# Performance work log

Hardware: AMD Instinct MI355X
Metric: run time of the kernel (lower is better)

Reference implementation:

```python
import jax, jax.numpy as jnp
import numpy as np

B, S, C, H, L = 256, 8, 8, 501, 56


def _lin_init(k, out_dim, in_dim):
    k1, k2 = jax.random.split(k)
    s = 1.0 / np.sqrt(in_dim)
    w = jax.random.uniform(k1, (out_dim, in_dim), jnp.float32, -s, s)
    b = jax.random.uniform(k2, (out_dim,), jnp.float32, -s, s)
    return w, b


def setup_inputs() -> dict:
    key = jax.random.key(0)
    ks = jax.random.split(key, 12)
    lin1_w, lin1_b = _lin_init(ks[0], H, L)
    av_w1, av_b1 = _lin_init(ks[1], 2 * H, H)
    av_w2, av_b2 = _lin_init(ks[2], C, 2 * H)
    ae_w1, ae_b1 = _lin_init(ks[3], 4 * H, 2 * H)
    ae_w2, ae_b2 = _lin_init(ks[4], 1, 4 * H)
    gate_w, gate_b = _lin_init(ks[5], H, H)
    map_w, map_b = _lin_init(ks[6], H, H)
    gru_w_ih, gru_b_ih = _lin_init(ks[7], 3 * H, C)
    gru_w_hh, gru_b_hh = _lin_init(ks[8], 3 * H, H)
    z = jax.random.normal(ks[9], (B, L), jnp.float32)
    dep_graph = jax.random.uniform(ks[10], (B, S, S), jnp.float32)
    node_encoding = jax.random.uniform(ks[11], (B, S, C), jnp.float32)
    return dict(z=z, dep_graph=dep_graph, node_encoding=node_encoding,
                lin1_w=lin1_w, lin1_b=lin1_b,
                av_w1=av_w1, av_b1=av_b1, av_w2=av_w2, av_b2=av_b2,
                ae_w1=ae_w1, ae_b1=ae_b1, ae_w2=ae_w2, ae_b2=ae_b2,
                gate_w=gate_w, gate_b=gate_b, map_w=map_w, map_b=map_b,
                gru_w_ih=gru_w_ih, gru_w_hh=gru_w_hh,
                gru_b_ih=gru_b_ih, gru_b_hh=gru_b_hh)


def _forward(z, dep_graph, node_encoding,
             lin1_w, lin1_b, av_w1, av_b1, av_w2, av_b2,
             ae_w1, ae_b1, ae_w2, ae_b2, gate_w, gate_b, map_w, map_b,
             gru_w_ih, gru_w_hh, gru_b_ih, gru_b_hh):
    b, s, _ = dep_graph.shape
    h = lin1_w.shape[0]

    def gru(x, hid):  # torch GRUCell math
        gi = x @ gru_w_ih.T + gru_b_ih
        gh = hid @ gru_w_hh.T + gru_b_hh
        i_r, i_z, i_n = jnp.split(gi, 3, axis=-1)
        h_r, h_z, h_n = jnp.split(gh, 3, axis=-1)
        r = jax.nn.sigmoid(i_r + h_r)
        zz = jax.nn.sigmoid(i_z + h_z)
        n = jnp.tanh(i_n + r * h_n)
        return (1.0 - zz) * n + zz * hid

    pos = jnp.arange(s)

    def outer_step(carry, xs):
        graph_state, nhs = carry  # (B,H), (B,S,H)
        index, x, dep_row = xs    # scalar, (B,C), (B,S)
        logits = jax.nn.softmax(
            jax.nn.relu(graph_state @ av_w1.T + av_b1) @ av_w2.T + av_b2, axis=-1)
        # index==0: gru seeded with graph_state; otherwise zero hidden
        h0 = jnp.where(index == 0, graph_state, jnp.zeros_like(graph_state))
        hv0 = gru(x, h0)

        def inner_step(c, j):
            hv, nhs_c, edge_row = c
            active = j < index  # replicate range(index-1, -1, -1)
            hidden_j = nhs_c[:, j]
            e = jnp.concatenate([hv, hidden_j], axis=1)
            edge = (jax.nn.relu(e @ ae_w1.T + ae_b1) @ ae_w2.T + ae_b2)[:, 0]
            edge_row = edge_row.at[:, j].set(jnp.where(active, edge, 0.0))
            # ancestors: dep_graph[:, index] with positions < j zeroed
            anc = dep_row * (pos >= j).astype(dep_row.dtype)
            a = (nhs_c * anc[:, :, None]).reshape(b * s, h)
            h_in = (jax.nn.sigmoid(a @ gate_w.T + gate_b) *
                    (a @ map_w.T + map_b)).reshape(b, s, h).sum(axis=1)
            hv_new = gru(x, h_in)
            hv = jnp.where(active, hv_new, hv)
            nhs_c = nhs_c.at[:, index].set(jnp.where(active, hv_new, nhs_c[:, index]))
            return (hv, nhs_c, edge_row), None

        (hv, nhs, edge_row), _ = jax.lax.scan(
            inner_step, (hv0, nhs, jnp.zeros((b, s), dep_graph.dtype)),
            jnp.arange(s - 1, -1, -1))
        nhs = nhs.at[:, index].set(hv)
        return (hv, nhs), (logits, edge_row)

    graph_state0 = z @ lin1_w.T + lin1_b
    nhs0 = jnp.zeros((b, s, h), z.dtype)
    (_, _), (gen_enc, gen_dep) = jax.lax.scan(
        outer_step, (graph_state0, nhs0),
        (jnp.arange(s), node_encoding.transpose(1, 0, 2), dep_graph.transpose(1, 0, 2)))
    return gen_dep.transpose(1, 0, 2), gen_enc.transpose(1, 0, 2)


def reference(z, dep_graph, node_encoding,
              lin1_w, lin1_b, av_w1, av_b1, av_w2, av_b2,
              ae_w1, ae_b1, ae_w2, ae_b2, gate_w, gate_b, map_w, map_b,
              gru_w_ih, gru_w_hh, gru_b_ih, gru_b_hh):
    return _forward(z, dep_graph, node_encoding,
                    lin1_w, lin1_b, av_w1, av_b1, av_w2, av_b2,
                    ae_w1, ae_b1, ae_w2, ae_b2, gate_w, gate_b, map_w, map_b,
                    gru_w_ih, gru_w_hh, gru_b_ih, gru_b_hh)
```

## Files before the change

kernel.cpp:

```cpp
#include <hip/hip_runtime.h>
#include <math.h>

constexpr int NB  = 256;
constexpr int NS  = 8;
constexpr int NC  = 8;
constexpr int NH  = 501;
constexpr int NL  = 56;
constexpr int NH2 = 1002;
constexpr int NH3 = 1503;
constexpr int NH4 = 2004;
constexpr int KT  = 1536;
constexpr int KE  = 512;
constexpr int HV  = 512 * 256;

typedef unsigned short u16;
typedef short bf16x8v __attribute__((ext_vector_type(8)));
typedef _Float16 f16x8v __attribute__((ext_vector_type(8)));
typedef _Float16 f16x4v __attribute__((ext_vector_type(4)));
typedef float f32x4 __attribute__((ext_vector_type(4)));

__device__ __forceinline__ float sigf(float x) { return 1.0f / (1.0f + __expf(-x)); }
__device__ __forceinline__ float tanh2(float x) { return 2.0f * sigf(2.0f * x) - 1.0f; }

__device__ __forceinline__ u16 f2bf(float x) {
  union { float f; unsigned u; } c; c.f = x;
  unsigned r = (c.u + 0x7fffu + ((c.u >> 16) & 1u)) >> 16;
  return (u16)r;
}
__device__ __forceinline__ float bf2f(u16 h) {
  union { float f; unsigned u; } c; c.u = ((unsigned)h) << 16; return c.f;
}

__device__ __forceinline__ void async_copy16(const void* g, void* l) {
  __builtin_amdgcn_global_load_lds(
      (const __attribute__((address_space(1))) unsigned int*)g,
      (__attribute__((address_space(3))) unsigned int*)l, 16, 0, 0);
}

__device__ __forceinline__ f32x4 mfma_bf(bf16x8v a, bf16x8v b, f32x4 c) {
  return __builtin_amdgcn_mfma_f32_16x16x32_bf16(a, b, c, 0, 0, 0);
}
__device__ __forceinline__ f32x4 mfma_h(f16x8v a, f16x8v b, f32x4 c) {
  return __builtin_amdgcn_mfma_f32_16x16x32_f16(a, b, c, 0, 0, 0);
}

__device__ __forceinline__ void storeTrio(u16* __restrict__ T, int b, int h0, const float v[4]) {
  size_t base = (size_t)b * KT;
  if (h0 + 3 < NH) {
    ushort4 hi4, lo4;
    u16 hi, lo;
    hi = f2bf(v[0]); lo = f2bf(v[0] - bf2f(hi)); hi4.x = hi; lo4.x = lo;
    hi = f2bf(v[1]); lo = f2bf(v[1] - bf2f(hi)); hi4.y = hi; lo4.y = lo;
    hi = f2bf(v[2]); lo = f2bf(v[2] - bf2f(hi)); hi4.z = hi; lo4.z = lo;
    hi = f2bf(v[3]); lo = f2bf(v[3] - bf2f(hi)); hi4.w = hi; lo4.w = lo;
    *(ushort4*)&T[base + h0]        = hi4;
    *(ushort4*)&T[base + 512 + h0]  = lo4;
    *(ushort4*)&T[base + 1024 + h0] = hi4;
  } else {
    for (int r = 0; r < 4; ++r) {
      int h = h0 + r;
      if (h < NH) {
        u16 hi = f2bf(v[r]); u16 lo = f2bf(v[r] - bf2f(hi));
        T[base + h] = hi; T[base + 512 + h] = lo; T[base + 1024 + h] = hi;
      }
    }
  }
}


__global__ __launch_bounds__(256) void kZero4(float4* __restrict__ p, int n4) {
  int i = blockIdx.x * 256 + threadIdx.x;
  if (i < n4) p[i] = make_float4(0.f, 0.f, 0.f, 0.f);
}

__global__ __launch_bounds__(256) void kInit0(float* __restrict__ out0,
                                              const float* __restrict__ ae_b2) {
  int e = blockIdx.x * 256 + threadIdx.x;
  int b = e >> 6, r = e & 63;
  int i = r >> 3, jj = r & 7;
  out0[b * 64 + i * 8 + jj] = (jj < i) ? ae_b2[0] : 0.f;
}

__global__ __launch_bounds__(256) void kPack(
    const float* __restrict__ gate_w, const float* __restrict__ map_w,
    const float* __restrict__ w_hh, const float* __restrict__ av_w1,
    const float* __restrict__ ae_w1,
    u16* __restrict__ Wgm, u16* __restrict__ Whh, u16* __restrict__ Wav1,
    u16* __restrict__ Wr3, _Float16* __restrict__ Wl) {
  int r = blockIdx.x;
  for (int k = threadIdx.x; k < 512; k += 256) {
    if (r < 5632) {
      float v = 0.f; u16* dst; int rr;
      if (r < 1024) {
        int h = (r < 512) ? r : r - 512;
        if (h < NH && k < NH) v = (r < 512) ? gate_w[h * NH + k] : map_w[h * NH + k];
        dst = Wgm; rr = r;
      } else if (r < 2560) {
        rr = r - 1024; int g = rr >> 9, h = rr & 511;
        if (h < NH && k < NH) v = w_hh[((size_t)g * NH + h) * NH + k];
        dst = Whh;
      } else if (r < 3584) {
        rr = r - 2560;
        if (rr < NH2 && k < NH) v = av_w1[(size_t)rr * NH + k];
        dst = Wav1;
      } else {
        rr = r - 3584;
        if (rr < NH4 && k < NH) v = ae_w1[(size_t)rr * NH2 + NH + k];
        dst = Wr3;
      }
      u16 hi = f2bf(v); u16 lo = f2bf(v - bf2f(hi));
      dst[(size_t)rr * KT + k] = hi;
      dst[(size_t)rr * KT + 512 + k] = hi;
      dst[(size_t)rr * KT + 1024 + k] = lo;
    } else {
      int m = r - 5632; float v = 0.f;
      if (m < NH4 && k < NH) v = ae_w1[(size_t)m * NH2 + k];
      Wl[(size_t)m * KE + k] = (_Float16)v;
    }
  }
}

__global__ __launch_bounds__(256) void kLin1(const float* __restrict__ z,
                                             const float* __restrict__ w,
                                             const float* __restrict__ bias,
                                             float* __restrict__ g0, u16* __restrict__ GS0) {
  int b = blockIdx.x;
  const float* zr = z + (size_t)b * NL;
  for (int h = threadIdx.x; h < NH; h += 256) {
    const float* wr = w + (size_t)h * NL;
    float acc = bias[h];
#pragma unroll
    for (int l = 0; l < NL; ++l) acc += zr[l] * wr[l];
    g0[h * NB + b] = acc;
    u16 hi = f2bf(acc), lo = f2bf(acc - bf2f(hi));
    GS0[(size_t)b * KT + h] = hi;
    GS0[(size_t)b * KT + 512 + h] = lo;
    GS0[(size_t)b * KT + 1024 + h] = hi;
  }
}

__global__ __launch_bounds__(256) void kGiAll(const float* __restrict__ ne,
                                              const float* __restrict__ w_ih,
                                              const float* __restrict__ b_ih,
                                              float* __restrict__ gi,
                                              float* __restrict__ giT) {
  int r = blockIdx.x, b = threadIdx.x;
  int g = (r >= NH2) ? 2 : ((r >= NH) ? 1 : 0);
  int h = r - g * NH;
  float wv[8];
#pragma unroll
  for (int c = 0; c < 8; ++c) wv[c] = w_ih[r * NC + c];
  float bb = b_ih[r];
  for (int idx = 0; idx < 8; ++idx) {
    float acc = bb;
#pragma unroll
    for (int c = 0; c < 8; ++c) acc += ne[b * 64 + idx * 8 + c] * wv[c];
    gi[((size_t)idx * NH3 + r) * NB + b] = acc;
    giT[((size_t)idx * NB + b) * KT + g * 512 + h] = acc;
  }
}


__global__ __launch_bounds__(256) void kGMw(
    const u16* __restrict__ Wgm, const u16* __restrict__ Bsrc, int mode,
    int index, int j, const float* __restrict__ dep,
    const float* __restrict__ gate_b, const float* __restrict__ map_b,
    const float* __restrict__ Pcj, const float* __restrict__ Qcj,
    float* __restrict__ RS, float* __restrict__ hinF, u16* __restrict__ hinT,
    float* __restrict__ PcO, float* __restrict__ QcO) {
  __shared__ f32x4 red[4 * 4 * 64];
  const int b = blockIdx.x, t = threadIdx.x, w = t >> 6, l = t & 63;
  const int quad = l >> 4, lan = l & 15;
  const int ht = b & 31, ct = b >> 5;
  const u16* Ag = Wgm + (size_t)(ht * 16 + lan) * KT;
  const u16* Am = Wgm + (size_t)(512 + ht * 16 + lan) * KT;
  const u16* B0 = Bsrc + (size_t)(ct * 32 + lan) * KT;
  const u16* B1 = Bsrc + (size_t)(ct * 32 + 16 + lan) * KT;
  const int kb = w * 384 + quad * 8;
  f32x4 a0 = {0.f,0.f,0.f,0.f}, a1 = a0, a2 = a0, a3 = a0;
#pragma unroll 4
  for (int ks = 0; ks < 12; ++ks) {
    int k = kb + ks * 32;
    bf16x8v bg = *(const bf16x8v*)&B0[k];
    bf16x8v bh = *(const bf16x8v*)&B1[k];
    bf16x8v ag = *(const bf16x8v*)&Ag[k];
    bf16x8v am = *(const bf16x8v*)&Am[k];
    a0 = mfma_bf(ag, bg, a0); a1 = mfma_bf(ag, bh, a1);
    a2 = mfma_bf(am, bg, a2); a3 = mfma_bf(am, bh, a3);
  }
  red[(w * 4 + 0) * 64 + l] = a0;
  red[(w * 4 + 1) * 64 + l] = a1;
  red[(w * 4 + 2) * 64 + l] = a2;
  red[(w * 4 + 3) * 64 + l] = a3;
  __syncthreads();
  if (w < 2) {
    int ns = w;
    f32x4 G = red[(0 * 4 + ns) * 64 + l] + red[(1 * 4 + ns) * 64 + l] +
              red[(2 * 4 + ns) * 64 + l] + red[(3 * 4 + ns) * 64 + l];
    f32x4 M = red[(0 * 4 + 2 + ns) * 64 + l] + red[(1 * 4 + 2 + ns) * 64 + l] +
              red[(2 * 4 + 2 + ns) * 64 + l] + red[(3 * 4 + 2 + ns) * 64 + l];
    int c = ct * 32 + ns * 16 + lan;
    int h0 = ht * 16 + quad * 4;
    if (mode == 1) {
#pragma unroll
      for (int reg = 0; reg < 4; ++reg) {
        int h = h0 + reg;
        if (h < NH) { PcO[h * NB + c] = G[reg]; QcO[h * NB + c] = M[reg]; }
      }
    } else {
      float dj = dep[c * 64 + index * 8 + j];
      float di = dep[c * 64 + index * 8 + index];
      float cnt = (float)(7 - (index - j));
      float vout[4];
#pragma unroll
      for (int reg = 0; reg < 4; ++reg) {
        int h = h0 + reg; float v = 0.f;
        if (h < NH) {
          float gb = gate_b[h], mb = map_b[h];
          float kbv = sigf(gb) * mb;
          float fj = sigf(dj * Pcj[h * NB + c] + gb) * (dj * Qcj[h * NB + c] + mb);
          float rs = RS[h * NB + c] + fj;
          RS[h * NB + c] = rs;
          float fi = sigf(di * G[reg] + gb) * (di * M[reg] + mb);
          v = rs + fi + cnt * kbv;
          hinF[h * NB + c] = v;
        }
        vout[reg] = v;
      }
      storeTrio(hinT, c, h0, vout);
    }
  }
}

__global__ __launch_bounds__(256) void kHHw(
    const u16* __restrict__ Whh, const u16* __restrict__ Bsrc,
    const float* __restrict__ hidF, const float* __restrict__ gi,
    const float* __restrict__ b_hh,
    u16* __restrict__ dstT, _Float16* __restrict__ XeSlot) {
  __shared__ f32x4 red[4 * 6 * 64];
  const int b = blockIdx.x, t = threadIdx.x, w = t >> 6, l = t & 63;
  const int quad = l >> 4, lan = l & 15;
  const int ht = b & 31, ct = b >> 5;
  const u16* Ar = Whh + (size_t)(ht * 16 + lan) * KT;
  const u16* Az = Whh + (size_t)(512 + ht * 16 + lan) * KT;
  const u16* An = Whh + (size_t)(1024 + ht * 16 + lan) * KT;
  const u16* B0 = Bsrc + (size_t)(ct * 32 + lan) * KT;
  const u16* B1 = Bsrc + (size_t)(ct * 32 + 16 + lan) * KT;
  const int kb = w * 384 + quad * 8;
  f32x4 r0 = {0.f,0.f,0.f,0.f}, r1 = r0, z0 = r0, z1 = r0, n0 = r0, n1 = r0;
#pragma unroll 4
  for (int ks = 0; ks < 12; ++ks) {
    int k = kb + ks * 32;
    bf16x8v bg = *(const bf16x8v*)&B0[k];
    bf16x8v bh = *(const bf16x8v*)&B1[k];
    bf16x8v ar = *(const bf16x8v*)&Ar[k];
    bf16x8v az = *(const bf16x8v*)&Az[k];
    bf16x8v an = *(const bf16x8v*)&An[k];
    r0 = mfma_bf(ar, bg, r0); r1 = mfma_bf(ar, bh, r1);
    z0 = mfma_bf(az, bg, z0); z1 = mfma_bf(az, bh, z1);
    n0 = mfma_bf(an, bg, n0); n1 = mfma_bf(an, bh, n1);
  }
  red[(w * 6 + 0) * 64 + l] = r0;
  red[(w * 6 + 1) * 64 + l] = r1;
  red[(w * 6 + 2) * 64 + l] = z0;
  red[(w * 6 + 3) * 64 + l] = z1;
  red[(w * 6 + 4) * 64 + l] = n0;
  red[(w * 6 + 5) * 64 + l] = n1;
  __syncthreads();
  if (w < 2) {
    int ns = w;
    f32x4 Rr = red[(0 * 6 + 0 + ns) * 64 + l] + red[(1 * 6 + 0 + ns) * 64 + l] +
               red[(2 * 6 + 0 + ns) * 64 + l] + red[(3 * 6 + 0 + ns) * 64 + l];
    f32x4 Rz = red[(0 * 6 + 2 + ns) * 64 + l] + red[(1 * 6 + 2 + ns) * 64 + l] +
               red[(2 * 6 + 2 + ns) * 64 + l] + red[(3 * 6 + 2 + ns) * 64 + l];
    f32x4 Rn = red[(0 * 6 + 4 + ns) * 64 + l] + red[(1 * 6 + 4 + ns) * 64 + l] +
               red[(2 * 6 + 4 + ns) * 64 + l] + red[(3 * 6 + 4 + ns) * 64 + l];
    int c = ct * 32 + ns * 16 + lan;
    int h0 = ht * 16 + quad * 4;
    float vout[4];
#pragma unroll
    for (int reg = 0; reg < 4; ++reg) {
      int h = h0 + reg; float v = 0.f;
      if (h < NH) {
        float ir = gi[h * NB + c];
        float iz = gi[(NH + h) * NB + c];
        float inn = gi[(2 * NH + h) * NB + c];
        float rr = sigf(ir + Rr[reg] + b_hh[h]);
        float zz = sigf(iz + Rz[reg] + b_hh[NH + h]);
        float nn = tanh2(inn + rr * (Rn[reg] + b_hh[2 * NH + h]));
        float hd = hidF[h * NB + c];
        v = (1.f - zz) * nn + zz * hd;
      }
      vout[reg] = v;
    }
    storeTrio(dstT, c, h0, vout);
    if (XeSlot) {
      if (h0 + 3 < NH) {
        f16x4v xv; xv[0] = (_Float16)vout[0]; xv[1] = (_Float16)vout[1];
        xv[2] = (_Float16)vout[2]; xv[3] = (_Float16)vout[3];
        *(f16x4v*)&XeSlot[(size_t)c * KE + h0] = xv;
      } else {
        for (int reg = 0; reg < 4; ++reg)
          if (h0 + reg < NH) XeSlot[(size_t)c * KE + h0 + reg] = (_Float16)vout[reg];
      }
    }
  }
}

__global__ __launch_bounds__(256) void kPRO(
    int index, const float* __restrict__ dep,
    const float* __restrict__ gate_b, const float* __restrict__ map_b,
    const float* __restrict__ Pcj, const float* __restrict__ Qcj,
    float* __restrict__ RS, float* __restrict__ hinF, u16* __restrict__ hinT,
    const float* __restrict__ giT, const float* __restrict__ b_hh,
    _Float16* __restrict__ Xe0) {
  const int b = blockIdx.x, t = threadIdx.x;
  const int j = index - 1;
  const float cnt = (float)(7 - (index - j));
  if (b < 251) {
#pragma unroll
    for (int hh = 0; hh < 2; ++hh) {
      int h = 2 * b + hh;
      if (h < NH) {
        int c = t;
        float gb = gate_b[h], mb = map_b[h];
        float kbv = sigf(gb) * mb;
        float dj = dep[c * 64 + index * 8 + j];
        float fj = sigf(dj * Pcj[h * NB + c] + gb) * (dj * Qcj[h * NB + c] + mb);
        RS[h * NB + c] = fj;
        float v = fj + kbv + cnt * kbv;
        hinF[h * NB + c] = v;
        u16 hi = f2bf(v), lo = f2bf(v - bf2f(hi));
        hinT[(size_t)c * KT + h] = hi;
        hinT[(size_t)c * KT + 512 + h] = lo;
        hinT[(size_t)c * KT + 1024 + h] = hi;
      }
    }
  }
  {
    int c = b;
    const float* g = giT + ((size_t)index * NB + c) * KT;
    for (int h = t; h < NH; h += 256) {
      float rr = sigf(g[h] + b_hh[h]);
      float zz = sigf(g[512 + h] + b_hh[NH + h]);
      float nn = tanh2(g[1024 + h] + rr * b_hh[2 * NH + h]);
      Xe0[(size_t)c * KE + h] = (_Float16)((1.f - zz) * nn);
    }
  }
}


__global__ __launch_bounds__(256) void kR(const u16* __restrict__ Wr3,
                                          const u16* __restrict__ Bsrc,
                                          _Float16* __restrict__ R) {
  __shared__ u16 sA[2][128 * 32];
  __shared__ u16 sB[2][128 * 32];
  const int t = threadIdx.x, w = t >> 6, l = t & 63, quad = l >> 4, lan = l & 15;
  const int mB = blockIdx.x * 128, nB0 = blockIdx.y * 128;
  const int qs = quad ^ ((lan >> 1) & 3);
  const int sseg = (l & 3) ^ ((l >> 3) & 3);
  const u16 *gA0, *gA1, *gB0, *gB1;
  {
    int r0 = (w * 2 + 0) * 16 + (l >> 2), r1 = (w * 2 + 1) * 16 + (l >> 2);
    gA0 = Wr3 + (size_t)(mB + r0) * KT + sseg * 8;
    gA1 = Wr3 + (size_t)(mB + r1) * KT + sseg * 8;
    gB0 = Bsrc + (size_t)(nB0 + r0) * KT + sseg * 8;
    gB1 = Bsrc + (size_t)(nB0 + r1) * KT + sseg * 8;
  }
  f32x4 acc[2][8];
#pragma unroll
  for (int mt = 0; mt < 2; ++mt)
#pragma unroll
    for (int ns = 0; ns < 8; ++ns) acc[mt][ns] = (f32x4){0.f,0.f,0.f,0.f};
  async_copy16(gA0, &sA[0][(w * 2 + 0) * 512]);
  async_copy16(gA1, &sA[0][(w * 2 + 1) * 512]);
  async_copy16(gB0, &sB[0][(w * 2 + 0) * 512]);
  async_copy16(gB1, &sB[0][(w * 2 + 1) * 512]);
  for (int c = 0; c < 48; ++c) {
    __syncthreads();
    if (c + 1 < 48) {
      int nb = (c + 1) & 1, off = (c + 1) * 32;
      async_copy16(gA0 + off, &sA[nb][(w * 2 + 0) * 512]);
      async_copy16(gA1 + off, &sA[nb][(w * 2 + 1) * 512]);
      async_copy16(gB0 + off, &sB[nb][(w * 2 + 0) * 512]);
      async_copy16(gB1 + off, &sB[nb][(w * 2 + 1) * 512]);
    }
    const u16* bufA = sA[c & 1];
    const u16* bufB = sB[c & 1];
    bf16x8v av[2];
#pragma unroll
    for (int mt = 0; mt < 2; ++mt)
      av[mt] = *(const bf16x8v*)&bufA[(w * 32 + mt * 16 + lan) * 32 + qs * 8];
#pragma unroll
    for (int ns = 0; ns < 8; ++ns) {
      bf16x8v bv = *(const bf16x8v*)&bufB[(ns * 16 + lan) * 32 + qs * 8];
#pragma unroll
      for (int mt = 0; mt < 2; ++mt) acc[mt][ns] = mfma_bf(av[mt], bv, acc[mt][ns]);
    }
  }
#pragma unroll
  for (int ns = 0; ns < 8; ++ns) {
    int col = nB0 + ns * 16 + lan;
#pragma unroll
    for (int mt = 0; mt < 2; ++mt) {
      int m0 = mB + w * 32 + mt * 16 + quad * 4;
      f16x4v rv;
#pragma unroll
      for (int reg = 0; reg < 4; ++reg) rv[reg] = (_Float16)acc[mt][ns][reg];
      *(f16x4v*)&R[(size_t)col * 2048 + m0] = rv;
    }
  }
}

__global__ __launch_bounds__(256) void kEdge(const _Float16* __restrict__ Wl,
                                             const _Float16* __restrict__ Xe,
                                             const _Float16* __restrict__ R,
                                             const float* __restrict__ ae_b1,
                                             const float* __restrict__ ae_w2,
                                             float* __restrict__ out0) {
  __shared__ u16 sA[2][128 * 32];
  __shared__ u16 sB[2][128 * 32];
  __shared__ float shW[4][8][16];
  const int t = threadIdx.x, w = t >> 6, l = t & 63, quad = l >> 4, lan = l & 15;
  const int mB = blockIdx.x * 128, nB0 = blockIdx.y * 128;
  const int qs = quad ^ ((lan >> 1) & 3);
  const int sseg = (l & 3) ^ ((l >> 3) & 3);
  int sid = blockIdx.y >> 1;
  int idec = 1, bse = 0;
  while (sid >= bse + idec) { bse += idec; idec++; }
  int jdec = idec - 1 - (sid - bse);
  const _Float16 *gA0, *gA1, *gB0, *gB1;
  {
    int r0 = (w * 2 + 0) * 16 + (l >> 2), r1 = (w * 2 + 1) * 16 + (l >> 2);
    gA0 = Wl + (size_t)(mB + r0) * KE + sseg * 8;
    gA1 = Wl + (size_t)(mB + r1) * KE + sseg * 8;
    gB0 = Xe + (size_t)(nB0 + r0) * KE + sseg * 8;
    gB1 = Xe + (size_t)(nB0 + r1) * KE + sseg * 8;
  }
  f32x4 acc[2][8];
#pragma unroll
  for (int mt = 0; mt < 2; ++mt)
#pragma unroll
    for (int ns = 0; ns < 8; ++ns) acc[mt][ns] = (f32x4){0.f,0.f,0.f,0.f};
  async_copy16(gA0, &sA[0][(w * 2 + 0) * 512]);
  async_copy16(gA1, &sA[0][(w * 2 + 1) * 512]);
  async_copy16(gB0, &sB[0][(w * 2 + 0) * 512]);
  async_copy16(gB1, &sB[0][(w * 2 + 1) * 512]);
  for (int c = 0; c < 16; ++c) {
    __syncthreads();
    if (c + 1 < 16) {
      int nb = (c + 1) & 1, off = (c + 1) * 32;
      async_copy16(gA0 + off, &sA[nb][(w * 2 + 0) * 512]);
      async_copy16(gA1 + off, &sA[nb][(w * 2 + 1) * 512]);
      async_copy16(gB0 + off, &sB[nb][(w * 2 + 0) * 512]);
      async_copy16(gB1 + off, &sB[nb][(w * 2 + 1) * 512]);
    }
    const u16* bufA = sA[c & 1];
    const u16* bufB = sB[c & 1];
    f16x8v av[2];
#pragma unroll
    for (int mt = 0; mt < 2; ++mt)
      av[mt] = *(const f16x8v*)&bufA[(w * 32 + mt * 16 + lan) * 32 + qs * 8];
#pragma unroll
    for (int ns = 0; ns < 8; ++ns) {
      f16x8v bv = *(const f16x8v*)&bufB[(ns * 16 + lan) * 32 + qs * 8];
#pragma unroll
      for (int mt = 0; mt < 2; ++mt) acc[mt][ns] = mfma_h(av[mt], bv, acc[mt][ns]);
    }
  }
  float b1v[2][4], w2v[2][4];
#pragma unroll
  for (int mt = 0; mt < 2; ++mt) {
    int m0 = mB + w * 32 + mt * 16 + quad * 4;
#pragma unroll
    for (int reg = 0; reg < 4; ++reg) {
      int m = m0 + reg;
      b1v[mt][reg] = (m < NH4) ? ae_b1[m] : 0.f;
      w2v[mt][reg] = (m < NH4) ? ae_w2[m] : 0.f;
    }
  }
#pragma unroll
  for (int ns = 0; ns < 8; ++ns) {
    int bcol = (nB0 + ns * 16 + lan) & 255;
    const _Float16* Rp = R + (size_t)(jdec * 256 + bcol) * 2048 + mB + w * 32;
    float s = 0.f;
#pragma unroll
    for (int mt = 0; mt < 2; ++mt) {
      f16x4v rv = *(const f16x4v*)&Rp[mt * 16 + quad * 4];
#pragma unroll
      for (int reg = 0; reg < 4; ++reg) {
        float v = acc[mt][ns][reg] + (float)rv[reg] + b1v[mt][reg];
        if (v > 0.f) s += v * w2v[mt][reg];
      }
    }
    s += __shfl_xor(s, 16);
    s += __shfl_xor(s, 32);
    if (quad == 0) shW[w][ns][lan] = s;
  }
  __syncthreads();
  if (t < 128) {
    int ns = t >> 4, ln = t & 15;
    float tot = shW[0][ns][ln] + shW[1][ns][ln] + shW[2][ns][ln] + shW[3][ns][ln];
    int b = (nB0 + ln + ns * 16) & 255;
    atomicAdd(&out0[b * 64 + idec * 8 + jdec], tot);
  }
}

__global__ __launch_bounds__(256) void kLogA(const u16* __restrict__ Wav1,
                                             const u16* __restrict__ Bsrc,
                                             const float* __restrict__ av_b1,
                                             _Float16* __restrict__ t1) {
  __shared__ u16 sA[2][128 * 32];
  __shared__ u16 sB[2][128 * 32];
  const int t = threadIdx.x, w = t >> 6, l = t & 63, quad = l >> 4, lan = l & 15;
  const int mB = blockIdx.x * 128, nB0 = blockIdx.y * 128;
  const int qs = quad ^ ((lan >> 1) & 3);
  const int sseg = (l & 3) ^ ((l >> 3) & 3);
  const u16 *gA0, *gA1, *gB0, *gB1;
  {
    int r0 = (w * 2 + 0) * 16 + (l >> 2), r1 = (w * 2 + 1) * 16 + (l >> 2);
    gA0 = Wav1 + (size_t)(mB + r0) * KT + sseg * 8;
    gA1 = Wav1 + (size_t)(mB + r1) * KT + sseg * 8;
    gB0 = Bsrc + (size_t)(nB0 + r0) * KT + sseg * 8;
    gB1 = Bsrc + (size_t)(nB0 + r1) * KT + sseg * 8;
  }
  f32x4 acc[2][8];
#pragma unroll
  for (int mt = 0; mt < 2; ++mt)
#pragma unroll
    for (int ns = 0; ns < 8; ++ns) acc[mt][ns] = (f32x4){0.f,0.f,0.f,0.f};
  async_copy16(gA0, &sA[0][(w * 2 + 0) * 512]);
  async_copy16(gA1, &sA[0][(w * 2 + 1) * 512]);
  async_copy16(gB0, &sB[0][(w * 2 + 0) * 512]);
  async_copy16(gB1, &sB[0][(w * 2 + 1) * 512]);
  for (int c = 0; c < 48; ++c) {
    __syncthreads();
    if (c + 1 < 48) {
      int nb = (c + 1) & 1, off = (c + 1) * 32;
      async_copy16(gA0 + off, &sA[nb][(w * 2 + 0) * 512]);
      async_copy16(gA1 + off, &sA[nb][(w * 2 + 1) * 512]);
      async_copy16(gB0 + off, &sB[nb][(w * 2 + 0) * 512]);
      async_copy16(gB1 + off, &sB[nb][(w * 2 + 1) * 512]);
    }
    const u16* bufA = sA[c & 1];
    const u16* bufB = sB[c & 1];
    bf16x8v av[2];
#pragma unroll
    for (int mt = 0; mt < 2; ++mt)
      av[mt] = *(const bf16x8v*)&bufA[(w * 32 + mt * 16 + lan) * 32 + qs * 8];
#pragma unroll
    for (int ns = 0; ns < 8; ++ns) {
      bf16x8v bv = *(const bf16x8v*)&bufB[(ns * 16 + lan) * 32 + qs * 8];
#pragma unroll
      for (int mt = 0; mt < 2; ++mt) acc[mt][ns] = mfma_bf(av[mt], bv, acc[mt][ns]);
    }
  }
#pragma unroll
  for (int ns = 0; ns < 8; ++ns) {
    int col = nB0 + ns * 16 + lan;
#pragma unroll
    for (int mt = 0; mt < 2; ++mt) {
      int m0 = mB + w * 32 + mt * 16 + quad * 4;
      f16x4v rv;
#pragma unroll
      for (int reg = 0; reg < 4; ++reg) {
        int m = m0 + reg;
        float v = acc[mt][ns][reg] + ((m < NH2) ? av_b1[m] : 0.f);
        rv[reg] = (_Float16)(v > 0.f ? v : 0.f);
      }
      *(f16x4v*)&t1[(size_t)col * 1024 + m0] = rv;
    }
  }
}

__global__ __launch_bounds__(256) void kSoft(const _Float16* __restrict__ t1,
                                             const float* __restrict__ av_w2,
                                             const float* __restrict__ av_b2,
                                             float* __restrict__ out1) {
  const int t = threadIdx.x, w = t >> 6, l = t & 63;
  int col = blockIdx.x * 4 + w;
  const _Float16* trow = t1 + (size_t)col * 1024;
  float s[8] = {};
  for (int i = 0; i < 16; ++i) {
    int k = i * 64 + l;
    if (k < NH2) {
      float v = (float)trow[k];
#pragma unroll
      for (int c = 0; c < 8; ++c) s[c] += v * av_w2[c * NH2 + k];
    }
  }
#pragma unroll
  for (int c = 0; c < 8; ++c) {
    s[c] += __shfl_xor(s[c], 32);
    s[c] += __shfl_xor(s[c], 16);
    s[c] += __shfl_xor(s[c], 8);
    s[c] += __shfl_xor(s[c], 4);
    s[c] += __shfl_xor(s[c], 2);
    s[c] += __shfl_xor(s[c], 1);
  }
  if (l == 0) {
    float lg[8], mx = -1e30f;
#pragma unroll
    for (int c = 0; c < 8; ++c) { lg[c] = s[c] + av_b2[c]; mx = fmaxf(mx, lg[c]); }
    float den = 0.f;
#pragma unroll
    for (int c = 0; c < 8; ++c) den += __expf(lg[c] - mx);
    int idx = col >> 8, b = col & 255;
#pragma unroll
    for (int c = 0; c < 8; ++c)
      out1[(b * NS + idx) * NC + c] = __expf(lg[c] - mx) / den;
  }
}


extern "C" void kernel_launch(void* const* d_in, const int* in_sizes, int n_in,
                              void* d_out, int out_size, void* d_ws, size_t ws_size,
                              hipStream_t stream) {
  (void)in_sizes; (void)n_in; (void)out_size; (void)ws_size;
  const float* z      = (const float*)d_in[0];
  const float* dep    = (const float*)d_in[1];
  const float* ne     = (const float*)d_in[2];
  const float* lin1_w = (const float*)d_in[3];
  const float* lin1_b = (const float*)d_in[4];
  const float* av_w1  = (const float*)d_in[5];
  const float* av_b1  = (const float*)d_in[6];
  const float* av_w2  = (const float*)d_in[7];
  const float* av_b2  = (const float*)d_in[8];
  const float* ae_w1  = (const float*)d_in[9];
  const float* ae_b1  = (const float*)d_in[10];
  const float* ae_w2  = (const float*)d_in[11];
  const float* ae_b2  = (const float*)d_in[12];
  const float* gate_w = (const float*)d_in[13];
  const float* gate_b = (const float*)d_in[14];
  const float* map_w  = (const float*)d_in[15];
  const float* map_b  = (const float*)d_in[16];
  const float* w_ih   = (const float*)d_in[17];
  const float* w_hh   = (const float*)d_in[18];
  const float* b_ih   = (const float*)d_in[19];
  const float* b_hh   = (const float*)d_in[20];

  float* out0 = (float*)d_out;
  float* out1 = out0 + NB * NS * NS;

  const size_t SLOT = (size_t)NB * KT;
  char* base = (char*)d_ws;
  u16* GS3   = (u16*)base;
  u16* hv3a  = GS3 + 9 * SLOT;
  u16* hv3b  = GS3 + 10 * SLOT;
  u16* hinT  = GS3 + 11 * SLOT;
  _Float16* Xe = (_Float16*)(GS3 + 12 * SLOT);
  char* p = base + 16777216;
  u16* Wgm  = (u16*)p; p += (size_t)1024 * KT * 2;
  u16* Whh  = (u16*)p; p += (size_t)1536 * KT * 2;
  u16* Wav1 = (u16*)p; p += (size_t)1024 * KT * 2;
  u16* Wr3  = (u16*)p; p += (size_t)2048 * KT * 2;
  _Float16* Wl = (_Float16*)p; p += (size_t)2048 * KE * 2;
  _Float16* R  = (_Float16*)p; p += (size_t)2048 * 2048 * 2;
  _Float16* t1 = (_Float16*)p; p += (size_t)2048 * 1024 * 2;
  float* Pc  = (float*)p; p += (size_t)8 * HV * 4;
  float* Qc  = (float*)p; p += (size_t)8 * HV * 4;
  float* RS  = (float*)p; p += (size_t)HV * 4;
  float* hinF = (float*)p; p += (size_t)HV * 4;
  float* g0  = (float*)p; p += (size_t)HV * 4;
  float* giN = (float*)p; p += (size_t)8 * NH3 * NB * 4;
  float* giT = (float*)p; p += (size_t)8 * NB * KT * 4;

  kZero4<<<4096, 256, 0, stream>>>((float4*)GS3, 1048576);
  kPack<<<7680, 256, 0, stream>>>(gate_w, map_w, w_hh, av_w1, ae_w1, Wgm, Whh, Wav1, Wr3, Wl);
  kInit0<<<64, 256, 0, stream>>>(out0, ae_b2);
  kLin1<<<256, 256, 0, stream>>>(z, lin1_w, lin1_b, g0, GS3);
  kGiAll<<<NH3, 256, 0, stream>>>(ne, w_ih, b_ih, giN, giT);

  kHHw<<<256, 256, 0, stream>>>(Whh, GS3, g0, giN, b_hh, GS3 + 1 * SLOT, nullptr);
  kGMw<<<256, 256, 0, stream>>>(Wgm, GS3 + 1 * SLOT, 1, 0, 0, dep, gate_b, map_b,
                                nullptr, nullptr, RS, hinF, hinT,
                                Pc + 0 * (size_t)HV, Qc + 0 * (size_t)HV);
  for (int index = 1; index < 8; ++index) {
    const float* gi_i = giN + (size_t)index * NH3 * NB;
    int sid0 = index * (index - 1) / 2;
    kPRO<<<256, 256, 0, stream>>>(index, dep, gate_b, map_b,
                                  Pc + (size_t)(index - 1) * HV, Qc + (size_t)(index - 1) * HV,
                                  RS, hinF, hinT, giT, b_hh,
                                  Xe + (size_t)sid0 * NB * KE);
    u16* dst = (index - 1 == 0) ? (GS3 + (size_t)(index + 1) * SLOT) : hv3a;
    kHHw<<<256, 256, 0, stream>>>(Whh, hinT, hinF, gi_i, b_hh, dst,
        (index - 1 > 0) ? (Xe + (size_t)(sid0 + 1) * NB * KE) : nullptr);
    u16* prev = dst;
    int pp = 1;
    for (int j = index - 2; j >= 0; --j) {
      kGMw<<<256, 256, 0, stream>>>(Wgm, prev, 0, index, j, dep, gate_b, map_b,
                                    Pc + (size_t)j * HV, Qc + (size_t)j * HV,
                                    RS, hinF, hinT, nullptr, nullptr);
      u16* d2 = (j == 0) ? (GS3 + (size_t)(index + 1) * SLOT) : (pp ? hv3b : hv3a);
      kHHw<<<256, 256, 0, stream>>>(Whh, hinT, hinF, gi_i, b_hh, d2,
          (j > 0) ? (Xe + (size_t)(sid0 + index - j) * NB * KE) : nullptr);
      prev = d2; pp ^= 1;
    }
    if (index < 7) {
      kGMw<<<256, 256, 0, stream>>>(Wgm, GS3 + (size_t)(index + 1) * SLOT, 1, 0, 0,
                                    dep, gate_b, map_b, nullptr, nullptr,
                                    RS, hinF, hinT,
                                    Pc + (size_t)index * HV, Qc + (size_t)index * HV);
    }
  }

  kR<<<dim3(16, 16), 256, 0, stream>>>(Wr3, GS3 + 1 * SLOT, R);
  kEdge<<<dim3(16, 56), 256, 0, stream>>>(Wl, Xe, R, ae_b1, ae_w2, out0);
  kLogA<<<dim3(8, 16), 256, 0, stream>>>(Wav1, GS3, av_b1, t1);
  kSoft<<<512, 256, 0, stream>>>(t1, av_w2, av_b2, out1);
}
```

Before: 942.1 us.

## Fuse init kernels, merge prologue into GM GEMM, drop R precompute in edge path

Merges the zeroing, lin1, gi and output-init kernels into one launch and zeroes only padding instead of whole buffers. The per-step prologue is fused into a new GM kernel that also computes the gated input. The hidden state is now recovered from the bf16 trio instead of a separate float buffer. The separate R GEMM is dropped: kEdge now uses a concatenated fp16 weight over both halves of ae_w1 plus stored node states Xn. kLogA tiling is also halved per block. These changes cut launches and intermediate traffic, at the cost of a larger K in the edge GEMM and slight precision differences in the hidden-state reconstruction.

```diff
diff --git a/kernel.cpp b/kernel.cpp
--- a/kernel.cpp
+++ b/kernel.cpp
@@ -11,6 +11,7 @@
 constexpr int NH4 = 2004;
 constexpr int KT  = 1536;
 constexpr int KE  = 512;
+constexpr int KA  = 1024;
 constexpr int HV  = 512 * 256;
 
 typedef unsigned short u16;
@@ -67,29 +68,15 @@
   }
 }
 
-
-__global__ __launch_bounds__(256) void kZero4(float4* __restrict__ p, int n4) {
-  int i = blockIdx.x * 256 + threadIdx.x;
-  if (i < n4) p[i] = make_float4(0.f, 0.f, 0.f, 0.f);
-}
-
-__global__ __launch_bounds__(256) void kInit0(float* __restrict__ out0,
-                                              const float* __restrict__ ae_b2) {
-  int e = blockIdx.x * 256 + threadIdx.x;
-  int b = e >> 6, r = e & 63;
-  int i = r >> 3, jj = r & 7;
-  out0[b * 64 + i * 8 + jj] = (jj < i) ? ae_b2[0] : 0.f;
-}
-
 __global__ __launch_bounds__(256) void kPack(
     const float* __restrict__ gate_w, const float* __restrict__ map_w,
     const float* __restrict__ w_hh, const float* __restrict__ av_w1,
     const float* __restrict__ ae_w1,
     u16* __restrict__ Wgm, u16* __restrict__ Whh, u16* __restrict__ Wav1,
-    u16* __restrict__ Wr3, _Float16* __restrict__ Wl) {
+    _Float16* __restrict__ Wlr) {
   int r = blockIdx.x;
-  for (int k = threadIdx.x; k < 512; k += 256) {
-    if (r < 5632) {
+  if (r < 3584) {
+    for (int k = threadIdx.x; k < 512; k += 256) {
       float v = 0.f; u16* dst; int rr;
       if (r < 1024) {
         int h = (r < 512) ? r : r - 512;
@@ -99,75 +86,97 @@
         rr = r - 1024; int g = rr >> 9, h = rr & 511;
         if (h < NH && k < NH) v = w_hh[((size_t)g * NH + h) * NH + k];
         dst = Whh;
-      } else if (r < 3584) {
+      } else {
         rr = r - 2560;
         if (rr < NH2 && k < NH) v = av_w1[(size_t)rr * NH + k];
         dst = Wav1;
-      } else {
-        rr = r - 3584;
-        if (rr < NH4 && k < NH) v = ae_w1[(size_t)rr * NH2 + NH + k];
-        dst = Wr3;
       }
       u16 hi = f2bf(v); u16 lo = f2bf(v - bf2f(hi));
       dst[(size_t)rr * KT + k] = hi;
       dst[(size_t)rr * KT + 512 + k] = hi;
       dst[(size_t)rr * KT + 1024 + k] = lo;
-    } else {
-      int m = r - 5632; float v = 0.f;
-      if (m < NH4 && k < NH) v = ae_w1[(size_t)m * NH2 + k];
-      Wl[(size_t)m * KE + k] = (_Float16)v;
-    }
-  }
-}
-
-__global__ __launch_bounds__(256) void kLin1(const float* __restrict__ z,
-                                             const float* __restrict__ w,
-                                             const float* __restrict__ bias,
-                                             float* __restrict__ g0, u16* __restrict__ GS0) {
-  int b = blockIdx.x;
-  const float* zr = z + (size_t)b * NL;
-  for (int h = threadIdx.x; h < NH; h += 256) {
-    const float* wr = w + (size_t)h * NL;
-    float acc = bias[h];
-#pragma unroll
-    for (int l = 0; l < NL; ++l) acc += zr[l] * wr[l];
-    g0[h * NB + b] = acc;
-    u16 hi = f2bf(acc), lo = f2bf(acc - bf2f(hi));
-    GS0[(size_t)b * KT + h] = hi;
-    GS0[(size_t)b * KT + 512 + h] = lo;
-    GS0[(size_t)b * KT + 1024 + h] = hi;
-  }
-}
-
-__global__ __launch_bounds__(256) void kGiAll(const float* __restrict__ ne,
-                                              const float* __restrict__ w_ih,
-                                              const float* __restrict__ b_ih,
-                                              float* __restrict__ gi,
-                                              float* __restrict__ giT) {
-  int r = blockIdx.x, b = threadIdx.x;
-  int g = (r >= NH2) ? 2 : ((r >= NH) ? 1 : 0);
-  int h = r - g * NH;
-  float wv[8];
-#pragma unroll
-  for (int c = 0; c < 8; ++c) wv[c] = w_ih[r * NC + c];
-  float bb = b_ih[r];
-  for (int idx = 0; idx < 8; ++idx) {
-    float acc = bb;
-#pragma unroll
-    for (int c = 0; c < 8; ++c) acc += ne[b * 64 + idx * 8 + c] * wv[c];
-    gi[((size_t)idx * NH3 + r) * NB + b] = acc;
-    giT[((size_t)idx * NB + b) * KT + g * 512 + h] = acc;
-  }
-}
-
-
-__global__ __launch_bounds__(256) void kGMw(
-    const u16* __restrict__ Wgm, const u16* __restrict__ Bsrc, int mode,
-    int index, int j, const float* __restrict__ dep,
-    const float* __restrict__ gate_b, const float* __restrict__ map_b,
-    const float* __restrict__ Pcj, const float* __restrict__ Qcj,
-    float* __restrict__ RS, float* __restrict__ hinF, u16* __restrict__ hinT,
-    float* __restrict__ PcO, float* __restrict__ QcO) {
+    }
+  } else {
+    int m = r - 3584;
+    for (int k = threadIdx.x; k < KA; k += 256) {
+      float v = 0.f;
+      if (m < NH4) {
+        if (k < 512) { if (k < NH) v = ae_w1[(size_t)m * NH2 + k]; }
+        else { int kk = k - 512; if (kk < NH) v = ae_w1[(size_t)m * NH2 + NH + kk]; }
+      }
+      Wlr[(size_t)m * KA + k] = (_Float16)v;
+    }
+  }
+}
+
+__global__ __launch_bounds__(256) void kInit(
+    float* __restrict__ out0, const float* __restrict__ ae_b2,
+    u16* __restrict__ trio, _Float16* __restrict__ Xe, _Float16* __restrict__ Xn,
+    const float* __restrict__ z, const float* __restrict__ lin1_w,
+    const float* __restrict__ lin1_b, float* __restrict__ g0,
+    const float* __restrict__ ne, const float* __restrict__ w_ih,
+    const float* __restrict__ b_ih, float* __restrict__ giN, float* __restrict__ giT) {
+  int blk = blockIdx.x, t = threadIdx.x;
+  if (blk < 64) {
+    int e = blk * 256 + t;
+    int b = e >> 6, r = e & 63;
+    int i = r >> 3, jj = r & 7;
+    out0[b * 64 + i * 8 + jj] = (jj < i) ? ae_b2[0] : 0.f;
+  } else if (blk < 75) {
+    u16* T = trio + (size_t)(blk - 64) * ((size_t)NB * KT) + (size_t)t * KT;
+#pragma unroll
+    for (int seg = 0; seg < 3; ++seg)
+      for (int h = NH; h < 512; ++h) T[seg * 512 + h] = 0;
+  } else if (blk < 103) {
+    _Float16* X = Xe + (size_t)(blk - 75) * NB * KE + (size_t)t * KE;
+    for (int h = NH; h < 512; ++h) X[h] = (_Float16)0.f;
+  } else if (blk < 110) {
+    _Float16* X = Xn + (size_t)(blk - 103) * NB * KE + (size_t)t * KE;
+    for (int h = NH; h < 512; ++h) X[h] = (_Float16)0.f;
+  } else if (blk < 366) {
+    int b = blk - 110;
+    const float* zr = z + (size_t)b * NL;
+    for (int h = t; h < NH; h += 256) {
+      const float* wr = lin1_w + (size_t)h * NL;
+      float acc = lin1_b[h];
+#pragma unroll
+      for (int l = 0; l < NL; ++l) acc += zr[l] * wr[l];
+      g0[h * NB + b] = acc;
+      u16 hi = f2bf(acc), lo = f2bf(acc - bf2f(hi));
+      trio[(size_t)b * KT + h] = hi;
+      trio[(size_t)b * KT + 512 + h] = lo;
+      trio[(size_t)b * KT + 1024 + h] = hi;
+    }
+  } else {
+    int r0 = (blk - 366) * 6, b = t;
+    for (int rr = 0; rr < 6; ++rr) {
+      int r = r0 + rr;
+      if (r >= NH3) break;
+      int g = (r >= NH2) ? 2 : ((r >= NH) ? 1 : 0);
+      int h = r - g * NH;
+      float wv[8];
+#pragma unroll
+      for (int c = 0; c < 8; ++c) wv[c] = w_ih[r * NC + c];
+      float bb = b_ih[r];
+      for (int idx = 0; idx < 8; ++idx) {
+        float acc = bb;
+#pragma unroll
+        for (int c = 0; c < 8; ++c) acc += ne[b * 64 + idx * 8 + c] * wv[c];
+        giN[((size_t)idx * NH3 + r) * NB + b] = acc;
+        giT[((size_t)idx * NB + b) * KT + g * 512 + h] = acc;
+      }
+    }
+  }
+}
+
+
+__global__ __launch_bounds__(256) void kGMT(
+    const u16* __restrict__ Wgm, const u16* __restrict__ Bsrc,
+    float* __restrict__ PcO, float* __restrict__ QcO,
+    const float* __restrict__ dep, const float* __restrict__ gate_b,
+    const float* __restrict__ map_b, float* __restrict__ RS, u16* __restrict__ hinT,
+    const float* __restrict__ giT, const float* __restrict__ b_hh,
+    _Float16* __restrict__ Xe0, int index) {
   __shared__ f32x4 red[4 * 4 * 64];
   const int b = blockIdx.x, t = threadIdx.x, w = t >> 6, l = t & 63;
   const int quad = l >> 4, lan = l & 15;
@@ -201,34 +210,100 @@
               red[(2 * 4 + 2 + ns) * 64 + l] + red[(3 * 4 + 2 + ns) * 64 + l];
     int c = ct * 32 + ns * 16 + lan;
     int h0 = ht * 16 + quad * 4;
-    if (mode == 1) {
-#pragma unroll
-      for (int reg = 0; reg < 4; ++reg) {
-        int h = h0 + reg;
-        if (h < NH) { PcO[h * NB + c] = G[reg]; QcO[h * NB + c] = M[reg]; }
-      }
-    } else {
-      float dj = dep[c * 64 + index * 8 + j];
-      float di = dep[c * 64 + index * 8 + index];
-      float cnt = (float)(7 - (index - j));
-      float vout[4];
-#pragma unroll
-      for (int reg = 0; reg < 4; ++reg) {
-        int h = h0 + reg; float v = 0.f;
-        if (h < NH) {
-          float gb = gate_b[h], mb = map_b[h];
-          float kbv = sigf(gb) * mb;
-          float fj = sigf(dj * Pcj[h * NB + c] + gb) * (dj * Qcj[h * NB + c] + mb);
-          float rs = RS[h * NB + c] + fj;
-          RS[h * NB + c] = rs;
-          float fi = sigf(di * G[reg] + gb) * (di * M[reg] + mb);
-          v = rs + fi + cnt * kbv;
-          hinF[h * NB + c] = v;
-        }
-        vout[reg] = v;
-      }
-      storeTrio(hinT, c, h0, vout);
-    }
+    int j = index - 1;
+    float dj = dep[c * 64 + index * 8 + j];
+    float vout[4];
+#pragma unroll
+    for (int reg = 0; reg < 4; ++reg) {
+      int h = h0 + reg; float v = 0.f;
+      if (h < NH) {
+        PcO[h * NB + c] = G[reg];
+        QcO[h * NB + c] = M[reg];
+        float gb = gate_b[h], mb = map_b[h];
+        float kbv = sigf(gb) * mb;
+        float fj = sigf(dj * G[reg] + gb) * (dj * M[reg] + mb);
+        RS[h * NB + c] = fj;
+        v = fj + 7.0f * kbv;
+      }
+      vout[reg] = v;
+    }
+    storeTrio(hinT, c, h0, vout);
+  } else {
+    int t2 = t - 128;
+    int c = ct * 32 + (t2 & 31);
+    int hb = t2 >> 5;
+    const float* g = giT + ((size_t)index * NB + c) * KT;
+#pragma unroll
+    for (int k = 0; k < 4; ++k) {
+      int h = ht * 16 + hb * 4 + k;
+      if (h < NH) {
+        float rr = sigf(g[h] + b_hh[h]);
+        float zz = sigf(g[512 + h] + b_hh[NH + h]);
+        float nn = tanh2(g[1024 + h] + rr * b_hh[2 * NH + h]);
+        Xe0[(size_t)c * KE + h] = (_Float16)((1.f - zz) * nn);
+      }
+    }
+  }
+}
+
+__global__ __launch_bounds__(256) void kGM0(
+    const u16* __restrict__ Wgm, const u16* __restrict__ Bsrc,
+    const float* __restrict__ dep, const float* __restrict__ gate_b,
+    const float* __restrict__ map_b,
+    const float* __restrict__ Pcj, const float* __restrict__ Qcj,
+    float* __restrict__ RS, u16* __restrict__ hinT, int index, int j) {
+  __shared__ f32x4 red[4 * 4 * 64];
+  const int b = blockIdx.x, t = threadIdx.x, w = t >> 6, l = t & 63;
+  const int quad = l >> 4, lan = l & 15;
+  const int ht = b & 31, ct = b >> 5;
+  const u16* Ag = Wgm + (size_t)(ht * 16 + lan) * KT;
+  const u16* Am = Wgm + (size_t)(512 + ht * 16 + lan) * KT;
+  const u16* B0 = Bsrc + (size_t)(ct * 32 + lan) * KT;
+  const u16* B1 = Bsrc + (size_t)(ct * 32 + 16 + lan) * KT;
+  const int kb = w * 384 + quad * 8;
+  f32x4 a0 = {0.f,0.f,0.f,0.f}, a1 = a0, a2 = a0, a3 = a0;
+#pragma unroll 4
+  for (int ks = 0; ks < 12; ++ks) {
+    int k = kb + ks * 32;
+    bf16x8v bg = *(const bf16x8v*)&B0[k];
+    bf16x8v bh = *(const bf16x8v*)&B1[k];
+    bf16x8v ag = *(const bf16x8v*)&Ag[k];
+    bf16x8v am = *(const bf16x8v*)&Am[k];
+    a0 = mfma_bf(ag, bg, a0); a1 = mfma_bf(ag, bh, a1);
+    a2 = mfma_bf(am, bg, a2); a3 = mfma_bf(am, bh, a3);
+  }
+  red[(w * 4 + 0) * 64 + l] = a0;
+  red[(w * 4 + 1) * 64 + l] = a1;
+  red[(w * 4 + 2) * 64 + l] = a2;
+  red[(w * 4 + 3) * 64 + l] = a3;
+  __syncthreads();
+  if (w < 2) {
+    int ns = w;
+    f32x4 G = red[(0 * 4 + ns) * 64 + l] + red[(1 * 4 + ns) * 64 + l] +
+              red[(2 * 4 + ns) * 64 + l] + red[(3 * 4 + ns) * 64 + l];
+    f32x4 M = red[(0 * 4 + 2 + ns) * 64 + l] + red[(1 * 4 + 2 + ns) * 64 + l] +
+              red[(2 * 4 + 2 + ns) * 64 + l] + red[(3 * 4 + 2 + ns) * 64 + l];
+    int c = ct * 32 + ns * 16 + lan;
+    int h0 = ht * 16 + quad * 4;
+    float dj = dep[c * 64 + index * 8 + j];
+    float di = dep[c * 64 + index * 8 + index];
+    float cnt = (float)(7 - (index - j));
+    float vout[4];
+#pragma unroll
+    for (int reg = 0; reg < 4; ++reg) {
+      int h = h0 + reg; float v = 0.f;
+      if (h < NH) {
+        float gb = gate_b[h], mb = map_b[h];
+        float kbv = sigf(gb) * mb;
+        float fj = sigf(dj * Pcj[h * NB + c] + gb) * (dj * Qcj[h * NB + c] + mb);
+        float rs = RS[h * NB + c] + fj;
+        RS[h * NB + c] = rs;
+        float fi = sigf(di * G[reg] + gb) * (di * M[reg] + mb);
+        v = rs + fi + cnt * kbv;
+      }
+      vout[reg] = v;
+    }
+    storeTrio(hinT, c, h0, vout);
   }
 }
 
@@ -236,7 +311,7 @@
     const u16* __restrict__ Whh, const u16* __restrict__ Bsrc,
     const float* __restrict__ hidF, const float* __restrict__ gi,
     const float* __restrict__ b_hh,
-    u16* __restrict__ dstT, _Float16* __restrict__ XeSlot) {
+    u16* __restrict__ dstT, _Float16* __restrict__ XeSlot, _Float16* __restrict__ XnSlot) {
   __shared__ f32x4 red[4 * 6 * 64];
   const int b = blockIdx.x, t = threadIdx.x, w = t >> 6, l = t & 63;
   const int quad = l >> 4, lan = l & 15;
@@ -288,133 +363,35 @@
         float rr = sigf(ir + Rr[reg] + b_hh[h]);
         float zz = sigf(iz + Rz[reg] + b_hh[NH + h]);
         float nn = tanh2(inn + rr * (Rn[reg] + b_hh[2 * NH + h]));
-        float hd = hidF[h * NB + c];
+        float hd;
+        if (hidF) hd = hidF[h * NB + c];
+        else hd = bf2f(Bsrc[(size_t)c * KT + h]) + bf2f(Bsrc[(size_t)c * KT + 512 + h]);
         v = (1.f - zz) * nn + zz * hd;
       }
       vout[reg] = v;
     }
     storeTrio(dstT, c, h0, vout);
-    if (XeSlot) {
+    if (XeSlot || XnSlot) {
       if (h0 + 3 < NH) {
         f16x4v xv; xv[0] = (_Float16)vout[0]; xv[1] = (_Float16)vout[1];
         xv[2] = (_Float16)vout[2]; xv[3] = (_Float16)vout[3];
-        *(f16x4v*)&XeSlot[(size_t)c * KE + h0] = xv;
+        if (XeSlot) *(f16x4v*)&XeSlot[(size_t)c * KE + h0] = xv;
+        if (XnSlot) *(f16x4v*)&XnSlot[(size_t)c * KE + h0] = xv;
       } else {
         for (int reg = 0; reg < 4; ++reg)
-          if (h0 + reg < NH) XeSlot[(size_t)c * KE + h0 + reg] = (_Float16)vout[reg];
-      }
-    }
-  }
-}
-
-__global__ __launch_bounds__(256) void kPRO(
-    int index, const float* __restrict__ dep,
-    const float* __restrict__ gate_b, const float* __restrict__ map_b,
-    const float* __restrict__ Pcj, const float* __restrict__ Qcj,
-    float* __restrict__ RS, float* __restrict__ hinF, u16* __restrict__ hinT,
-    const float* __restrict__ giT, const float* __restrict__ b_hh,
-    _Float16* __restrict__ Xe0) {
-  const int b = blockIdx.x, t = threadIdx.x;
-  const int j = index - 1;
-  const float cnt = (float)(7 - (index - j));
-  if (b < 251) {
-#pragma unroll
-    for (int hh = 0; hh < 2; ++hh) {
-      int h = 2 * b + hh;
-      if (h < NH) {
-        int c = t;
-        float gb = gate_b[h], mb = map_b[h];
-        float kbv = sigf(gb) * mb;
-        float dj = dep[c * 64 + index * 8 + j];
-        float fj = sigf(dj * Pcj[h * NB + c] + gb) * (dj * Qcj[h * NB + c] + mb);
-        RS[h * NB + c] = fj;
-        float v = fj + kbv + cnt * kbv;
-        hinF[h * NB + c] = v;
-        u16 hi = f2bf(v), lo = f2bf(v - bf2f(hi));
-        hinT[(size_t)c * KT + h] = hi;
-        hinT[(size_t)c * KT + 512 + h] = lo;
-        hinT[(size_t)c * KT + 1024 + h] = hi;
-      }
-    }
-  }
-  {
-    int c = b;
-    const float* g = giT + ((size_t)index * NB + c) * KT;
-    for (int h = t; h < NH; h += 256) {
-      float rr = sigf(g[h] + b_hh[h]);
-      float zz = sigf(g[512 + h] + b_hh[NH + h]);
-      float nn = tanh2(g[1024 + h] + rr * b_hh[2 * NH + h]);
-      Xe0[(size_t)c * KE + h] = (_Float16)((1.f - zz) * nn);
-    }
-  }
-}
-
-
-__global__ __launch_bounds__(256) void kR(const u16* __restrict__ Wr3,
-                                          const u16* __restrict__ Bsrc,
-                                          _Float16* __restrict__ R) {
-  __shared__ u16 sA[2][128 * 32];
-  __shared__ u16 sB[2][128 * 32];
-  const int t = threadIdx.x, w = t >> 6, l = t & 63, quad = l >> 4, lan = l & 15;
-  const int mB = blockIdx.x * 128, nB0 = blockIdx.y * 128;
-  const int qs = quad ^ ((lan >> 1) & 3);
-  const int sseg = (l & 3) ^ ((l >> 3) & 3);
-  const u16 *gA0, *gA1, *gB0, *gB1;
-  {
-    int r0 = (w * 2 + 0) * 16 + (l >> 2), r1 = (w * 2 + 1) * 16 + (l >> 2);
-    gA0 = Wr3 + (size_t)(mB + r0) * KT + sseg * 8;
-    gA1 = Wr3 + (size_t)(mB + r1) * KT + sseg * 8;
-    gB0 = Bsrc + (size_t)(nB0 + r0) * KT + sseg * 8;
-    gB1 = Bsrc + (size_t)(nB0 + r1) * KT + sseg * 8;
-  }
-  f32x4 acc[2][8];
-#pragma unroll
-  for (int mt = 0; mt < 2; ++mt)
-#pragma unroll
-    for (int ns = 0; ns < 8; ++ns) acc[mt][ns] = (f32x4){0.f,0.f,0.f,0.f};
-  async_copy16(gA0, &sA[0][(w * 2 + 0) * 512]);
-  async_copy16(gA1, &sA[0][(w * 2 + 1) * 512]);
-  async_copy16(gB0, &sB[0][(w * 2 + 0) * 512]);
-  async_copy16(gB1, &sB[0][(w * 2 + 1) * 512]);
-  for (int c = 0; c < 48; ++c) {
-    __syncthreads();
-    if (c + 1 < 48) {
-      int nb = (c + 1) & 1, off = (c + 1) * 32;
-      async_copy16(gA0 + off, &sA[nb][(w * 2 + 0) * 512]);
-      async_copy16(gA1 + off, &sA[nb][(w * 2 + 1) * 512]);
-      async_copy16(gB0 + off, &sB[nb][(w * 2 + 0) * 512]);
-      async_copy16(gB1 + off, &sB[nb][(w * 2 + 1) * 512]);
-    }
-    const u16* bufA = sA[c & 1];
-    const u16* bufB = sB[c & 1];
-    bf16x8v av[2];
-#pragma unroll
-    for (int mt = 0; mt < 2; ++mt)
-      av[mt] = *(const bf16x8v*)&bufA[(w * 32 + mt * 16 + lan) * 32 + qs * 8];
-#pragma unroll
-    for (int ns = 0; ns < 8; ++ns) {
-      bf16x8v bv = *(const bf16x8v*)&bufB[(ns * 16 + lan) * 32 + qs * 8];
-#pragma unroll
-      for (int mt = 0; mt < 2; ++mt) acc[mt][ns] = mfma_bf(av[mt], bv, acc[mt][ns]);
-    }
-  }
-#pragma unroll
-  for (int ns = 0; ns < 8; ++ns) {
-    int col = nB0 + ns * 16 + lan;
-#pragma unroll
-    for (int mt = 0; mt < 2; ++mt) {
-      int m0 = mB + w * 32 + mt * 16 + quad * 4;
-      f16x4v rv;
-#pragma unroll
-      for (int reg = 0; reg < 4; ++reg) rv[reg] = (_Float16)acc[mt][ns][reg];
-      *(f16x4v*)&R[(size_t)col * 2048 + m0] = rv;
-    }
-  }
-}
-
-__global__ __launch_bounds__(256) void kEdge(const _Float16* __restrict__ Wl,
+          if (h0 + reg < NH) {
+            if (XeSlot) XeSlot[(size_t)c * KE + h0 + reg] = (_Float16)vout[reg];
+            if (XnSlot) XnSlot[(size_t)c * KE + h0 + reg] = (_Float16)vout[reg];
+          }
+      }
+    }
+  }
+}
+
+
+__global__ __launch_bounds__(256) void kEdge(const _Float16* __restrict__ Wlr,
                                              const _Float16* __restrict__ Xe,
-                                             const _Float16* __restrict__ R,
+                                             const _Float16* __restrict__ Xn,
                                              const float* __restrict__ ae_b1,
                                              const float* __restrict__ ae_w2,
                                              float* __restrict__ out0) {
@@ -429,14 +406,13 @@
   int idec = 1, bse = 0;
   while (sid >= bse + idec) { bse += idec; idec++; }
   int jdec = idec - 1 - (sid - bse);
-  const _Float16 *gA0, *gA1, *gB0, *gB1;
-  {
-    int r0 = (w * 2 + 0) * 16 + (l >> 2), r1 = (w * 2 + 1) * 16 + (l >> 2);
-    gA0 = Wl + (size_t)(mB + r0) * KE + sseg * 8;
-    gA1 = Wl + (size_t)(mB + r1) * KE + sseg * 8;
-    gB0 = Xe + (size_t)(nB0 + r0) * KE + sseg * 8;
-    gB1 = Xe + (size_t)(nB0 + r1) * KE + sseg * 8;
-  }
+  int r0 = (w * 2 + 0) * 16 + (l >> 2), r1 = (w * 2 + 1) * 16 + (l >> 2);
+  const _Float16* gA0 = Wlr + (size_t)(mB + r0) * KA + sseg * 8;
+  const _Float16* gA1 = Wlr + (size_t)(mB + r1) * KA + sseg * 8;
+  const _Float16* Xe0 = Xe + (size_t)(nB0 + r0) * KE + sseg * 8;
+  const _Float16* Xe1 = Xe + (size_t)(nB0 + r1) * KE + sseg * 8;
+  const _Float16* Xn0 = Xn + ((size_t)jdec * NB + ((nB0 + r0) & 255)) * KE + sseg * 8;
+  const _Float16* Xn1 = Xn + ((size_t)jdec * NB + ((nB0 + r1) & 255)) * KE + sseg * 8;
   f32x4 acc[2][8];
 #pragma unroll
   for (int mt = 0; mt < 2; ++mt)
@@ -444,16 +420,18 @@
     for (int ns = 0; ns < 8; ++ns) acc[mt][ns] = (f32x4){0.f,0.f,0.f,0.f};
   async_copy16(gA0, &sA[0][(w * 2 + 0) * 512]);
   async_copy16(gA1, &sA[0][(w * 2 + 1) * 512]);
-  async_copy16(gB0, &sB[0][(w * 2 + 0) * 512]);
-  async_copy16(gB1, &sB[0][(w * 2 + 1) * 512]);
-  for (int c = 0; c < 16; ++c) {
+  async_copy16(Xe0, &sB[0][(w * 2 + 0) * 512]);
+  async_copy16(Xe1, &sB[0][(w * 2 + 1) * 512]);
+  for (int c = 0; c < 32; ++c) {
     __syncthreads();
-    if (c + 1 < 16) {
-      int nb = (c + 1) & 1, off = (c + 1) * 32;
-      async_copy16(gA0 + off, &sA[nb][(w * 2 + 0) * 512]);
-      async_copy16(gA1 + off, &sA[nb][(w * 2 + 1) * 512]);
-      async_copy16(gB0 + off, &sB[nb][(w * 2 + 0) * 512]);
-      async_copy16(gB1 + off, &sB[nb][(w * 2 + 1) * 512]);
+    if (c + 1 < 32) {
+      int nb = (c + 1) & 1, cc = c + 1;
+      async_copy16(gA0 + cc * 32, &sA[nb][(w * 2 + 0) * 512]);
+      async_copy16(gA1 + cc * 32, &sA[nb][(w * 2 + 1) * 512]);
+      const _Float16* b0 = (cc < 16) ? (Xe0 + cc * 32) : (Xn0 + (cc - 16) * 32);
+      const _Float16* b1 = (cc < 16) ? (Xe1 + cc * 32) : (Xn1 + (cc - 16) * 32);
+      async_copy16(b0, &sB[nb][(w * 2 + 0) * 512]);
+      async_copy16(b1, &sB[nb][(w * 2 + 1) * 512]);
     }
     const u16* bufA = sA[c & 1];
     const u16* bufB = sB[c & 1];
@@ -481,15 +459,12 @@
   }
 #pragma unroll
   for (int ns = 0; ns < 8; ++ns) {
-    int bcol = (nB0 + ns * 16 + lan) & 255;
-    const _Float16* Rp = R + (size_t)(jdec * 256 + bcol) * 2048 + mB + w * 32;
     float s = 0.f;
 #pragma unroll
     for (int mt = 0; mt < 2; ++mt) {
-      f16x4v rv = *(const f16x4v*)&Rp[mt * 16 + quad * 4];
 #pragma unroll
       for (int reg = 0; reg < 4; ++reg) {
-        float v = acc[mt][ns][reg] + (float)rv[reg] + b1v[mt][reg];
+        float v = acc[mt][ns][reg] + b1v[mt][reg];
         if (v > 0.f) s += v * w2v[mt][reg];
       }
     }
@@ -510,66 +485,52 @@
                                              const u16* __restrict__ Bsrc,
                                              const float* __restrict__ av_b1,
                                              _Float16* __restrict__ t1) {
-  __shared__ u16 sA[2][128 * 32];
+  __shared__ u16 sA[2][64 * 32];
   __shared__ u16 sB[2][128 * 32];
   const int t = threadIdx.x, w = t >> 6, l = t & 63, quad = l >> 4, lan = l & 15;
-  const int mB = blockIdx.x * 128, nB0 = blockIdx.y * 128;
+  const int mB = blockIdx.x * 64, nB0 = blockIdx.y * 128;
   const int qs = quad ^ ((lan >> 1) & 3);
   const int sseg = (l & 3) ^ ((l >> 3) & 3);
-  const u16 *gA0, *gA1, *gB0, *gB1;
-  {
-    int r0 = (w * 2 + 0) * 16 + (l >> 2), r1 = (w * 2 + 1) * 16 + (l >> 2);
-    gA0 = Wav1 + (size_t)(mB + r0) * KT + sseg * 8;
-    gA1 = Wav1 + (size_t)(mB + r1) * KT + sseg * 8;
-    gB0 = Bsrc + (size_t)(nB0 + r0) * KT + sseg * 8;
-    gB1 = Bsrc + (size_t)(nB0 + r1) * KT + sseg * 8;
-  }
-  f32x4 acc[2][8];
-#pragma unroll
-  for (int mt = 0; mt < 2; ++mt)
-#pragma unroll
-    for (int ns = 0; ns < 8; ++ns) acc[mt][ns] = (f32x4){0.f,0.f,0.f,0.f};
-  async_copy16(gA0, &sA[0][(w * 2 + 0) * 512]);
-  async_copy16(gA1, &sA[0][(w * 2 + 1) * 512]);
+  int rA = w * 16 + (l >> 2);
+  int r0 = (w * 2 + 0) * 16 + (l >> 2), r1 = (w * 2 + 1) * 16 + (l >> 2);
+  const u16* gA = Wav1 + (size_t)(mB + rA) * KT + sseg * 8;
+  const u16* gB0 = Bsrc + (size_t)(nB0 + r0) * KT + sseg * 8;
+  const u16* gB1 = Bsrc + (size_t)(nB0 + r1) * KT + sseg * 8;
+  f32x4 acc[8];
+#pragma unroll
+  for (int ns = 0; ns < 8; ++ns) acc[ns] = (f32x4){0.f,0.f,0.f,0.f};
+  async_copy16(gA, &sA[0][w * 512]);
   async_copy16(gB0, &sB[0][(w * 2 + 0) * 512]);
   async_copy16(gB1, &sB[0][(w * 2 + 1) * 512]);
   for (int c = 0; c < 48; ++c) {
     __syncthreads();
     if (c + 1 < 48) {
       int nb = (c + 1) & 1, off = (c + 1) * 32;
-      async_copy16(gA0 + off, &sA[nb][(w * 2 + 0) * 512]);
-      async_copy16(gA1 + off, &sA[nb][(w * 2 + 1) * 512]);
+      async_copy16(gA + off, &sA[nb][w * 512]);
       async_copy16(gB0 + off, &sB[nb][(w * 2 + 0) * 512]);
       async_copy16(gB1 + off, &sB[nb][(w * 2 + 1) * 512]);
     }
     const u16* bufA = sA[c & 1];
     const u16* bufB = sB[c & 1];
-    bf16x8v av[2];
-#pragma unroll
-    for (int mt = 0; mt < 2; ++mt)
-      av[mt] = *(const bf16x8v*)&bufA[(w * 32 + mt * 16 + lan) * 32 + qs * 8];
+    bf16x8v av = *(const bf16x8v*)&bufA[(w * 16 + lan) * 32 + qs * 8];
 #pragma unroll
     for (int ns = 0; ns < 8; ++ns) {
       bf16x8v bv = *(const bf16x8v*)&bufB[(ns * 16 + lan) * 32 + qs * 8];
-#pragma unroll
-      for (int mt = 0; mt < 2; ++mt) acc[mt][ns] = mfma_bf(av[mt], bv, acc[mt][ns]);
+      acc[ns] = mfma_bf(av, bv, acc[ns]);
     }
   }
 #pragma unroll
   for (int ns = 0; ns < 8; ++ns) {
     int col = nB0 + ns * 16 + lan;
-#pragma unroll
-    for (int mt = 0; mt < 2; ++mt) {
-      int m0 = mB + w * 32 + mt * 16 + quad * 4;
-      f16x4v rv;
-#pragma unroll
-      for (int reg = 0; reg < 4; ++reg) {
-        int m = m0 + reg;
-        float v = acc[mt][ns][reg] + ((m < NH2) ? av_b1[m] : 0.f);
-        rv[reg] = (_Float16)(v > 0.f ? v : 0.f);
-      }
-      *(f16x4v*)&t1[(size_t)col * 1024 + m0] = rv;
-    }
+    int m0 = mB + w * 16 + quad * 4;
+    f16x4v rv;
+#pragma unroll
+    for (int reg = 0; reg < 4; ++reg) {
+      int m = m0 + reg;
+      float v = acc[ns][reg] + ((m < NH2) ? av_b1[m] : 0.f);
+      rv[reg] = (_Float16)(v > 0.f ? v : 0.f);
+    }
+    *(f16x4v*)&t1[(size_t)col * 1024 + m0] = rv;
   }
 }
 
@@ -643,69 +604,61 @@
   float* out1 = out0 + NB * NS * NS;
 
   const size_t SLOT = (size_t)NB * KT;
-  char* base = (char*)d_ws;
-  u16* GS3   = (u16*)base;
-  u16* hv3a  = GS3 + 9 * SLOT;
-  u16* hv3b  = GS3 + 10 * SLOT;
-  u16* hinT  = GS3 + 11 * SLOT;
-  _Float16* Xe = (_Float16*)(GS3 + 12 * SLOT);
-  char* p = base + 16777216;
-  u16* Wgm  = (u16*)p; p += (size_t)1024 * KT * 2;
-  u16* Whh  = (u16*)p; p += (size_t)1536 * KT * 2;
-  u16* Wav1 = (u16*)p; p += (size_t)1024 * KT * 2;
-  u16* Wr3  = (u16*)p; p += (size_t)2048 * KT * 2;
-  _Float16* Wl = (_Float16*)p; p += (size_t)2048 * KE * 2;
-  _Float16* R  = (_Float16*)p; p += (size_t)2048 * 2048 * 2;
-  _Float16* t1 = (_Float16*)p; p += (size_t)2048 * 1024 * 2;
-  float* Pc  = (float*)p; p += (size_t)8 * HV * 4;
-  float* Qc  = (float*)p; p += (size_t)8 * HV * 4;
-  float* RS  = (float*)p; p += (size_t)HV * 4;
-  float* hinF = (float*)p; p += (size_t)HV * 4;
-  float* g0  = (float*)p; p += (size_t)HV * 4;
-  float* giN = (float*)p; p += (size_t)8 * NH3 * NB * 4;
-  float* giT = (float*)p; p += (size_t)8 * NB * KT * 4;
-
-  kZero4<<<4096, 256, 0, stream>>>((float4*)GS3, 1048576);
-  kPack<<<7680, 256, 0, stream>>>(gate_w, map_w, w_hh, av_w1, ae_w1, Wgm, Whh, Wav1, Wr3, Wl);
-  kInit0<<<64, 256, 0, stream>>>(out0, ae_b2);
-  kLin1<<<256, 256, 0, stream>>>(z, lin1_w, lin1_b, g0, GS3);
-  kGiAll<<<NH3, 256, 0, stream>>>(ne, w_ih, b_ih, giN, giT);
-
-  kHHw<<<256, 256, 0, stream>>>(Whh, GS3, g0, giN, b_hh, GS3 + 1 * SLOT, nullptr);
-  kGMw<<<256, 256, 0, stream>>>(Wgm, GS3 + 1 * SLOT, 1, 0, 0, dep, gate_b, map_b,
-                                nullptr, nullptr, RS, hinF, hinT,
-                                Pc + 0 * (size_t)HV, Qc + 0 * (size_t)HV);
-  for (int index = 1; index < 8; ++index) {
+  char* p = (char*)d_ws;
+  u16* trio = (u16*)p;            p += 11 * SLOT * 2;
+  _Float16* Xe = (_Float16*)p;    p += (size_t)28 * NB * KE * 2;
+  _Float16* Xn = (_Float16*)p;    p += (size_t)7 * NB * KE * 2;
+  u16* Wgm  = (u16*)p;            p += (size_t)1024 * KT * 2;
+  u16* Whh  = (u16*)p;            p += (size_t)1536 * KT * 2;
+  u16* Wav1 = (u16*)p;            p += (size_t)1024 * KT * 2;
+  _Float16* Wlr = (_Float16*)p;   p += (size_t)2048 * KA * 2;
+  _Float16* t1 = (_Float16*)p;    p += (size_t)2048 * 1024 * 2;
+  float* Pc   = (float*)p;        p += (size_t)8 * HV * 4;
+  float* Qc   = (float*)p;        p += (size_t)8 * HV * 4;
+  float* RS   = (float*)p;        p += (size_t)HV * 4;
+  float* g0   = (float*)p;        p += (size_t)HV * 4;
+  float* giN  = (float*)p;        p += (size_t)8 * NH3 * NB * 4;
+  float* giT  = (float*)p;        p += (size_t)8 * NB * KT * 4;
+
+  u16* hinT = trio + 8 * SLOT;
+
+  kPack<<<5632, 256, 0, stream>>>(gate_w, map_w, w_hh, av_w1, ae_w1, Wgm, Whh, Wav1, Wlr);
+  kInit<<<617, 256, 0, stream>>>(out0, ae_b2, trio, Xe, Xn,
+                                 z, lin1_w, lin1_b, g0, ne, w_ih, b_ih, giN, giT);
+
+  kHHw<<<256, 256, 0, stream>>>(Whh, trio, g0, giN, b_hh,
+                                trio + 1 * SLOT, nullptr, Xn);
+
+  for (int i = 0; i <= 6; ++i) {
+    int index = i + 1;
+    int sid0 = index * (index - 1) / 2;
     const float* gi_i = giN + (size_t)index * NH3 * NB;
-    int sid0 = index * (index - 1) / 2;
-    kPRO<<<256, 256, 0, stream>>>(index, dep, gate_b, map_b,
-                                  Pc + (size_t)(index - 1) * HV, Qc + (size_t)(index - 1) * HV,
-                                  RS, hinF, hinT, giT, b_hh,
-                                  Xe + (size_t)sid0 * NB * KE);
-    u16* dst = (index - 1 == 0) ? (GS3 + (size_t)(index + 1) * SLOT) : hv3a;
-    kHHw<<<256, 256, 0, stream>>>(Whh, hinT, hinF, gi_i, b_hh, dst,
-        (index - 1 > 0) ? (Xe + (size_t)(sid0 + 1) * NB * KE) : nullptr);
+    kGMT<<<256, 256, 0, stream>>>(Wgm, trio + (size_t)(i + 1) * SLOT,
+                                  Pc + (size_t)i * HV, Qc + (size_t)i * HV,
+                                  dep, gate_b, map_b, RS, hinT, giT, b_hh,
+                                  Xe + (size_t)sid0 * NB * KE, index);
+    bool final1 = (index == 1);
+    u16* dst = final1 ? (trio + 2 * SLOT) : (trio + 9 * SLOT);
+    kHHw<<<256, 256, 0, stream>>>(Whh, hinT, nullptr, gi_i, b_hh, dst,
+        (index - 1 > 0) ? (Xe + (size_t)(sid0 + 1) * NB * KE) : nullptr,
+        final1 ? (Xn + (size_t)1 * NB * KE) : nullptr);
     u16* prev = dst;
-    int pp = 1;
+    int par = 1;
     for (int j = index - 2; j >= 0; --j) {
-      kGMw<<<256, 256, 0, stream>>>(Wgm, prev, 0, index, j, dep, gate_b, map_b,
+      kGM0<<<256, 256, 0, stream>>>(Wgm, prev, dep, gate_b, map_b,
                                     Pc + (size_t)j * HV, Qc + (size_t)j * HV,
-                                    RS, hinF, hinT, nullptr, nullptr);
-      u16* d2 = (j == 0) ? (GS3 + (size_t)(index + 1) * SLOT) : (pp ? hv3b : hv3a);
-      kHHw<<<256, 256, 0, stream>>>(Whh, hinT, hinF, gi_i, b_hh, d2,
-          (j > 0) ? (Xe + (size_t)(sid0 + index - j) * NB * KE) : nullptr);
-      prev = d2; pp ^= 1;
-    }
-    if (index < 7) {
-      kGMw<<<256, 256, 0, stream>>>(Wgm, GS3 + (size_t)(index + 1) * SLOT, 1, 0, 0,
-                                    dep, gate_b, map_b, nullptr, nullptr,
-                                    RS, hinF, hinT,
-                                    Pc + (size_t)index * HV, Qc + (size_t)index * HV);
-    }
-  }
-
-  kR<<<dim3(16, 16), 256, 0, stream>>>(Wr3, GS3 + 1 * SLOT, R);
-  kEdge<<<dim3(16, 56), 256, 0, stream>>>(Wl, Xe, R, ae_b1, ae_w2, out0);
-  kLogA<<<dim3(8, 16), 256, 0, stream>>>(Wav1, GS3, av_b1, t1);
+                                    RS, hinT, index, j);
+      bool fin = (j == 0);
+      u16* d2 = (fin && index <= 6) ? (trio + (size_t)(index + 1) * SLOT)
+                                    : (trio + (size_t)(9 + par) * SLOT);
+      kHHw<<<256, 256, 0, stream>>>(Whh, hinT, nullptr, gi_i, b_hh, d2,
+          (j > 0) ? (Xe + (size_t)(sid0 + index - j) * NB * KE) : nullptr,
+          (fin && index <= 6) ? (Xn + (size_t)index * NB * KE) : nullptr);
+      prev = d2; par ^= 1;
+    }
+  }
+
+  kLogA<<<dim3(16, 16), 256, 0, stream>>>(Wav1, trio, av_b1, t1);
   kSoft<<<512, 256, 0, stream>>>(t1, av_w2, av_b2, out1);
-}
+  kEdge<<<dim3(16, 56), 256, 0, stream>>>(Wlr, Xe, Xn, ae_b1, ae_w2, out0);
+}
```

Result: faster. 879.3 us (-6.7%).
